# Performance work log

Hardware: AMD Instinct MI355X
Metric: run time of the kernel (lower is better)

Reference implementation:

```python
import jax, jax.numpy as jnp
import numpy as np

N_NODES = 50000
N_EDGES = 800000
D_FEAT = 64


def setup_inputs() -> dict:
    key = jax.random.key(0)
    k_x, k_e, k_w = jax.random.split(key, 3)
    x = jax.random.normal(k_x, (N_NODES, D_FEAT), dtype=jnp.float32)
    edge_index = jax.random.randint(k_e, (2, N_EDGES), 0, N_NODES, dtype=jnp.int64)
    # message MLP params (phi_Theta): single linear + ReLU
    W = jax.random.normal(k_w, (D_FEAT, D_FEAT), dtype=jnp.float32) / np.sqrt(D_FEAT)
    b = jnp.zeros((D_FEAT,), dtype=jnp.float32)
    return {"x": x, "edge_index": edge_index, "W": W, "b": b}


def reference(x, edge_index, W, b):
    # flow = source_to_target: messages flow from edge_index[0] (j) to edge_index[1] (i)
    src = edge_index[0]  # j: source nodes (gather)
    dst = edge_index[1]  # i: target nodes (scatter index)
    n_nodes = x.shape[0]
    # __collect__: index_select gather of source node features -> x_j [E, D]
    x_j = x[src]
    # message: per-edge MLP  phi(x_j) = relu(x_j W + b)
    msg = jax.nn.relu(jnp.einsum('ed,df->ef', x_j, W) + b)
    # aggregate: scatter-add into target nodes (aggr='add', dim_size = size_i)
    out = jax.ops.segment_sum(msg, dst, num_segments=n_nodes)
    # update: identity
    return out
```

## Files before the change

### kernel.cpp

```cpp
#include <hip/hip_runtime.h>
#include <hip/hip_bf16.h>

#define D 64
#define CAP 32
#define OVF_CAP 16384
#define TROWS 64


__device__ __forceinline__ float bf2f(unsigned short u) {
    return __uint_as_float((unsigned int)u << 16);
}
__device__ __forceinline__ unsigned short f2bf(float f) {
    unsigned int u = __float_as_uint(f);
    unsigned int r = (u + 0x7fffu + ((u >> 16) & 1u)) >> 16;
    return (unsigned short)r;
}

__global__ __launch_bounds__(256) void node_mlp_lds_kernel(
    const float* __restrict__ x, const float* __restrict__ W,
    const float* __restrict__ b, unsigned short* __restrict__ m,
    int* __restrict__ cnt, int* __restrict__ ovf_cnt, int n_nodes) {
    __shared__ float tile[TROWS][68];
    for (int i = blockIdx.x * blockDim.x + threadIdx.x; i < n_nodes;
         i += gridDim.x * blockDim.x) cnt[i] = 0;
    if (blockIdx.x == 0 && threadIdx.x == 0) *ovf_cnt = 0;

    const int lane = threadIdx.x & 63;
    const int wv = threadIdx.x >> 6;
    float w[D];
    #pragma unroll
    for (int k = 0; k < D; ++k) w[k] = W[k * D + lane];
    const float bias = b[lane];

    for (int t0 = blockIdx.x * TROWS; t0 < n_nodes; t0 += gridDim.x * TROWS) {
        const int nr = min(TROWS, n_nodes - t0);
        {
            const int r = threadIdx.x >> 2, sg = threadIdx.x & 3;
            if (r < nr) {
                const float4* s4 = (const float4*)(x + (size_t)(t0 + r) * D + sg * 16);
                float4 a0 = s4[0], a1 = s4[1], a2 = s4[2], a3 = s4[3];
                float* dl = &tile[r][sg * 16];
                *(float4*)(dl + 0)  = a0;
                *(float4*)(dl + 4)  = a1;
                *(float4*)(dl + 8)  = a2;
                *(float4*)(dl + 12) = a3;
            }
        }
        __syncthreads();
        const int rend = min(wv * 16 + 16, nr);
        for (int rr = wv * 16; rr < rend; rr += 2) {
            const int r0 = rr;
            const int r1 = (rr + 1 < rend) ? rr + 1 : rr;
            float acc0 = bias, acc1 = bias;
            #pragma unroll
            for (int kk = 0; kk < D / 4; ++kk) {
                float4 a = *(const float4*)&tile[r0][4 * kk];
                float4 c = *(const float4*)&tile[r1][4 * kk];
                acc0 = fmaf(a.x, w[4 * kk + 0], acc0);
                acc1 = fmaf(c.x, w[4 * kk + 0], acc1);
                acc0 = fmaf(a.y, w[4 * kk + 1], acc0);
                acc1 = fmaf(c.y, w[4 * kk + 1], acc1);
                acc0 = fmaf(a.z, w[4 * kk + 2], acc0);
                acc1 = fmaf(c.z, w[4 * kk + 2], acc1);
                acc0 = fmaf(a.w, w[4 * kk + 3], acc0);
                acc1 = fmaf(c.w, w[4 * kk + 3], acc1);
            }
            m[(size_t)(t0 + r0) * D + lane] = f2bf(fmaxf(acc0, 0.0f));
            if (r1 > r0)
                m[(size_t)(t0 + r1) * D + lane] = f2bf(fmaxf(acc1, 0.0f));
        }
        __syncthreads();
    }
}

__global__ __launch_bounds__(256) void append_kernel(
    const int* __restrict__ src, const int* __restrict__ dst,
    int* __restrict__ cnt, unsigned short* __restrict__ slots,
    int* __restrict__ ovf_cnt, unsigned int* __restrict__ ovf,
    int n_edges) {
    const int stride = gridDim.x * 256;
    for (int e = blockIdx.x * 256 + (int)threadIdx.x; e < n_edges; e += stride) {
        int d = dst[e];
        int s = src[e];
        int pos = atomicAdd(&cnt[d], 1);
        if (pos < CAP) {
            slots[(size_t)d * CAP + pos] = (unsigned short)s;
        } else {
            int op = atomicAdd(ovf_cnt, 1);
            if (op < OVF_CAP)
                ovf[op] = ((unsigned int)d << 16) | (unsigned int)s;
        }
    }
}

__global__ __launch_bounds__(256) void gather_kernel(
    const unsigned short* __restrict__ slots, const int* __restrict__ cnt,
    const unsigned short* __restrict__ m,
    const int* __restrict__ ovf_cnt, const unsigned int* __restrict__ ovf,
    float* __restrict__ out, int n_nodes) {
    const int grp = blockIdx.x >> 3;
    const int xcd = blockIdx.x & 7;
    int node = grp * 32 + ((threadIdx.x >> 6) << 3) + xcd;
    if (node >= n_nodes) return;
    node = __builtin_amdgcn_readfirstlane(node);

    const int lane = threadIdx.x & 63;

    const int c = cnt[node];
    const int cc = min(c, CAP);
    const unsigned int* __restrict__ row =
        (const unsigned int*)(slots + (size_t)node * CAP);

    float acc = 0.0f;
    int k = 0;
    for (; k + 16 <= cc; k += 16) {
        unsigned int p[8];
        #pragma unroll
        for (int i = 0; i < 8; ++i) p[i] = row[(k >> 1) + i];
        float v[16];
        #pragma unroll
        for (int i = 0; i < 8; ++i) {
            const unsigned short* ba = m + (size_t)(p[i] & 0xFFFFu) * D;
            const unsigned short* bb = m + (size_t)(p[i] >> 16) * D;
            v[2 * i + 0] = bf2f(ba[lane]);
            v[2 * i + 1] = bf2f(bb[lane]);
        }
        float t0 = ((v[0] + v[1]) + (v[2] + v[3])) + ((v[4] + v[5]) + (v[6] + v[7]));
        float t1 = ((v[8] + v[9]) + (v[10] + v[11])) + ((v[12] + v[13]) + (v[14] + v[15]));
        acc += t0 + t1;
    }
    for (; k + 4 <= cc; k += 4) {
        unsigned int p0 = row[(k >> 1) + 0];
        unsigned int p1 = row[(k >> 1) + 1];
        const unsigned short* b0 = m + (size_t)(p0 & 0xFFFFu) * D;
        const unsigned short* b1 = m + (size_t)(p0 >> 16) * D;
        const unsigned short* b2 = m + (size_t)(p1 & 0xFFFFu) * D;
        const unsigned short* b3 = m + (size_t)(p1 >> 16) * D;
        float v0 = bf2f(b0[lane]);
        float v1 = bf2f(b1[lane]);
        float v2 = bf2f(b2[lane]);
        float v3 = bf2f(b3[lane]);
        acc += (v0 + v1) + (v2 + v3);
    }
    for (; k < cc; ++k) {
        unsigned int p = row[k >> 1];
        unsigned int s = (k & 1) ? (p >> 16) : (p & 0xFFFFu);
        acc += bf2f(m[(size_t)s * D + lane]);
    }
    if (c > CAP) {
        int oc = min(*ovf_cnt, OVF_CAP);
        for (int i = 0; i < oc; ++i) {
            unsigned int e = ovf[i];
            if ((int)(e >> 16) == node)
                acc += bf2f(m[(size_t)(e & 0xFFFFu) * D + lane]);
        }
    }
    out[(size_t)node * D + lane] = acc;
}

__global__ __launch_bounds__(256) void edge_scatter_kernel(
    const int* __restrict__ src, const int* __restrict__ dst,
    const unsigned short* __restrict__ m, float* __restrict__ out, int n_edges) {
    long long t = (long long)blockIdx.x * blockDim.x + threadIdx.x;
    int e = (int)(t >> 4);
    if (e >= n_edges) return;
    int c = (int)(t & 15) << 2;
    int s = src[e];
    int d = dst[e];
    const ushort4 v = *(const ushort4*)(m + (size_t)s * D + c);
    float* o = out + (size_t)d * D + c;
    atomicAdd(o + 0, bf2f(v.x));
    atomicAdd(o + 1, bf2f(v.y));
    atomicAdd(o + 2, bf2f(v.z));
    atomicAdd(o + 3, bf2f(v.w));
}

static inline size_t align_up(size_t v, size_t a) { return (v + a - 1) & ~(a - 1); }

extern "C" void kernel_launch(void* const* d_in, const int* in_sizes, int n_in,
                              void* d_out, int out_size, void* d_ws, size_t ws_size,
                              hipStream_t stream) {
    const float* x = (const float*)d_in[0];
    const int* edge_index = (const int*)d_in[1];
    const float* W = (const float*)d_in[2];
    const float* b = (const float*)d_in[3];
    float* out = (float*)d_out;

    const int n_nodes = in_sizes[0] / D;
    const int n_edges = in_sizes[1] / 2;
    const int* src = edge_index;
    const int* dst = edge_index + n_edges;

    size_t off = 0;
    unsigned short* m = (unsigned short*)((char*)d_ws + off);
    off = align_up(off + (size_t)n_nodes * D * sizeof(unsigned short), 256);
    int* cnt = (int*)((char*)d_ws + off);
    off = align_up(off + (size_t)n_nodes * sizeof(int), 256);
    unsigned short* slots = (unsigned short*)((char*)d_ws + off);
    off = align_up(off + (size_t)n_nodes * CAP * sizeof(unsigned short), 256);
    int* ovf_cnt = (int*)((char*)d_ws + off);
    off = align_up(off + sizeof(int), 256);
    unsigned int* ovf = (unsigned int*)((char*)d_ws + off);
    off = align_up(off + (size_t)OVF_CAP * sizeof(unsigned int), 256);
    const size_t needed = off;

    const int mlp_blocks = (n_nodes + TROWS - 1) / TROWS;
    node_mlp_lds_kernel<<<mlp_blocks, 256, 0, stream>>>(x, W, b, m, cnt, ovf_cnt, n_nodes);

    if (ws_size >= needed && n_nodes <= 65536) {
        const int app_blocks = (n_edges + 255) / 256;
        append_kernel<<<app_blocks, 256, 0, stream>>>(
            src, dst, cnt, slots, ovf_cnt, ovf, n_edges);
        const int ngroups = (n_nodes + 31) / 32;
        gather_kernel<<<ngroups * 8, 256, 0, stream>>>(
            slots, cnt, m, ovf_cnt, ovf, out, n_nodes);
    } else {
        hipMemsetAsync(d_out, 0, (size_t)out_size * sizeof(float), stream);
        long long total_threads = (long long)n_edges * 16;
        int scat_blocks = (int)((total_threads + 255) / 256);
        edge_scatter_kernel<<<scat_blocks, 256, 0, stream>>>(src, dst, m, out, n_edges);
    }
}
```

Baseline: 150.5 us.

## Shard append kernel by destination node modulo XCD count

The append kernel is restructured so each block handles one of eight destination shards (dst mod 8), matching the blockIdx-to-XCD mapping. The goal is to keep the atomics on cnt and the slot writes for a node inside one XCD's L2, avoiding cross-die coherence traffic. It also unrolls four edges per thread so more atomics are in flight at once. The cost is that every shard reads the whole dst array, which multiplies index reads by eight, and each thread gets fewer useful edges.

```diff
diff --git a/kernel.cpp b/kernel.cpp
--- a/kernel.cpp
+++ b/kernel.cpp
@@ -4,6 +4,7 @@
 #define D 64
 #define CAP 32
 #define OVF_CAP 16384
+#define NSHARD 8
 #define TROWS 64
 
 
@@ -77,18 +78,39 @@
     const int* __restrict__ src, const int* __restrict__ dst,
     int* __restrict__ cnt, unsigned short* __restrict__ slots,
     int* __restrict__ ovf_cnt, unsigned int* __restrict__ ovf,
-    int n_edges) {
-    const int stride = gridDim.x * 256;
-    for (int e = blockIdx.x * 256 + (int)threadIdx.x; e < n_edges; e += stride) {
-        int d = dst[e];
-        int s = src[e];
-        int pos = atomicAdd(&cnt[d], 1);
-        if (pos < CAP) {
-            slots[(size_t)d * CAP + pos] = (unsigned short)s;
-        } else {
-            int op = atomicAdd(ovf_cnt, 1);
-            if (op < OVF_CAP)
-                ovf[op] = ((unsigned int)d << 16) | (unsigned int)s;
+    int n_edges, int blocks_per_shard) {
+    const int shard = blockIdx.x & (NSHARD - 1);
+    const int p = blockIdx.x >> 3;
+    const int chunk = (n_edges + blocks_per_shard - 1) / blocks_per_shard;
+    const int beg = p * chunk;
+    const int end = min(beg + chunk, n_edges);
+
+    for (int e0 = beg + (int)threadIdx.x; e0 < end; e0 += 256 * 4) {
+        int  dd[4], ss[4];
+        bool mm[4];
+        #pragma unroll
+        for (int u = 0; u < 4; ++u) {
+            const int e = e0 + u * 256;
+            const bool valid = (e < end);
+            const int d = valid ? dst[e] : 0;
+            mm[u] = valid && ((d & (NSHARD - 1)) == shard);
+            dd[u] = d;
+            ss[u] = mm[u] ? src[e] : 0;
+        }
+        int pos[4];
+        #pragma unroll
+        for (int u = 0; u < 4; ++u)
+            if (mm[u]) pos[u] = atomicAdd(&cnt[dd[u]], 1);
+        #pragma unroll
+        for (int u = 0; u < 4; ++u) {
+            if (!mm[u]) continue;
+            if (pos[u] < CAP) {
+                slots[(size_t)dd[u] * CAP + pos[u]] = (unsigned short)ss[u];
+            } else {
+                int op = atomicAdd(ovf_cnt, 1);
+                if (op < OVF_CAP)
+                    ovf[op] = ((unsigned int)dd[u] << 16) | (unsigned int)ss[u];
+            }
         }
     }
 }
@@ -208,9 +230,9 @@
     node_mlp_lds_kernel<<<mlp_blocks, 256, 0, stream>>>(x, W, b, m, cnt, ovf_cnt, n_nodes);
 
     if (ws_size >= needed && n_nodes <= 65536) {
-        const int app_blocks = (n_edges + 255) / 256;
-        append_kernel<<<app_blocks, 256, 0, stream>>>(
-            src, dst, cnt, slots, ovf_cnt, ovf, n_edges);
+        const int blocks_per_shard = 320;
+        append_kernel<<<blocks_per_shard * NSHARD, 256, 0, stream>>>(
+            src, dst, cnt, slots, ovf_cnt, ovf, n_edges, blocks_per_shard);
         const int ngroups = (n_nodes + 31) / 32;
         gather_kernel<<<ngroups * 8, 256, 0, stream>>>(
             slots, cnt, m, ovf_cnt, ovf, out, n_nodes);
```

Measured after the change: 144.2 us. 1.04x faster.

## Shard edge append by destination XCD and retile node MLP to 32 rows

Applied to the files above, without the earlier changes.

The append kernel now assigns each block to a shard (blockIdx & 7), matching the round-robin block-to-XCD dispatch. Each block scans a chunk of edges and keeps only those whose destination node falls in its shard, so the atomics and slot writes for a node stay within one XCD's L2. The price is that every edge's dst is read 8 times across shards. The node MLP separately switches to 32-row tiles with 4 rows per wave iteration, giving more blocks and more ILP per wave.

```diff
diff --git a/kernel.cpp b/kernel.cpp
--- a/kernel.cpp
+++ b/kernel.cpp
@@ -4,7 +4,8 @@
 #define D 64
 #define CAP 32
 #define OVF_CAP 16384
-#define TROWS 64
+#define NSHARD 8
+#define TROWS 32
 
 
 __device__ __forceinline__ float bf2f(unsigned short u) {
@@ -35,39 +36,50 @@
     for (int t0 = blockIdx.x * TROWS; t0 < n_nodes; t0 += gridDim.x * TROWS) {
         const int nr = min(TROWS, n_nodes - t0);
         {
-            const int r = threadIdx.x >> 2, sg = threadIdx.x & 3;
+            const int r = threadIdx.x >> 3, sg = threadIdx.x & 7;
             if (r < nr) {
-                const float4* s4 = (const float4*)(x + (size_t)(t0 + r) * D + sg * 16);
-                float4 a0 = s4[0], a1 = s4[1], a2 = s4[2], a3 = s4[3];
-                float* dl = &tile[r][sg * 16];
-                *(float4*)(dl + 0)  = a0;
-                *(float4*)(dl + 4)  = a1;
-                *(float4*)(dl + 8)  = a2;
-                *(float4*)(dl + 12) = a3;
+                const float4* s4 = (const float4*)(x + (size_t)(t0 + r) * D + sg * 8);
+                float4 a0 = s4[0], a1 = s4[1];
+                float* dl = &tile[r][sg * 8];
+                *(float4*)(dl + 0) = a0;
+                *(float4*)(dl + 4) = a1;
             }
         }
         __syncthreads();
-        const int rend = min(wv * 16 + 16, nr);
-        for (int rr = wv * 16; rr < rend; rr += 2) {
+        const int rend = min(wv * 8 + 8, nr);
+        for (int rr = wv * 8; rr < rend; rr += 4) {
             const int r0 = rr;
-            const int r1 = (rr + 1 < rend) ? rr + 1 : rr;
-            float acc0 = bias, acc1 = bias;
+            const int r1 = min(rr + 1, rend - 1);
+            const int r2 = min(rr + 2, rend - 1);
+            const int r3 = min(rr + 3, rend - 1);
+            float acc0 = bias, acc1 = bias, acc2 = bias, acc3 = bias;
             #pragma unroll
             for (int kk = 0; kk < D / 4; ++kk) {
                 float4 a = *(const float4*)&tile[r0][4 * kk];
                 float4 c = *(const float4*)&tile[r1][4 * kk];
+                float4 e = *(const float4*)&tile[r2][4 * kk];
+                float4 g = *(const float4*)&tile[r3][4 * kk];
                 acc0 = fmaf(a.x, w[4 * kk + 0], acc0);
                 acc1 = fmaf(c.x, w[4 * kk + 0], acc1);
+                acc2 = fmaf(e.x, w[4 * kk + 0], acc2);
+                acc3 = fmaf(g.x, w[4 * kk + 0], acc3);
                 acc0 = fmaf(a.y, w[4 * kk + 1], acc0);
                 acc1 = fmaf(c.y, w[4 * kk + 1], acc1);
+                acc2 = fmaf(e.y, w[4 * kk + 1], acc2);
+                acc3 = fmaf(g.y, w[4 * kk + 1], acc3);
                 acc0 = fmaf(a.z, w[4 * kk + 2], acc0);
                 acc1 = fmaf(c.z, w[4 * kk + 2], acc1);
+                acc2 = fmaf(e.z, w[4 * kk + 2], acc2);
+                acc3 = fmaf(g.z, w[4 * kk + 2], acc3);
                 acc0 = fmaf(a.w, w[4 * kk + 3], acc0);
                 acc1 = fmaf(c.w, w[4 * kk + 3], acc1);
+                acc2 = fmaf(e.w, w[4 * kk + 3], acc2);
+                acc3 = fmaf(g.w, w[4 * kk + 3], acc3);
             }
             m[(size_t)(t0 + r0) * D + lane] = f2bf(fmaxf(acc0, 0.0f));
-            if (r1 > r0)
-                m[(size_t)(t0 + r1) * D + lane] = f2bf(fmaxf(acc1, 0.0f));
+            if (rr + 1 < rend) m[(size_t)(t0 + r1) * D + lane] = f2bf(fmaxf(acc1, 0.0f));
+            if (rr + 2 < rend) m[(size_t)(t0 + r2) * D + lane] = f2bf(fmaxf(acc2, 0.0f));
+            if (rr + 3 < rend) m[(size_t)(t0 + r3) * D + lane] = f2bf(fmaxf(acc3, 0.0f));
         }
         __syncthreads();
     }
@@ -77,10 +89,16 @@
     const int* __restrict__ src, const int* __restrict__ dst,
     int* __restrict__ cnt, unsigned short* __restrict__ slots,
     int* __restrict__ ovf_cnt, unsigned int* __restrict__ ovf,
-    int n_edges) {
-    const int stride = gridDim.x * 256;
-    for (int e = blockIdx.x * 256 + (int)threadIdx.x; e < n_edges; e += stride) {
+    int n_edges, int blocks_per_shard) {
+    const int shard = blockIdx.x & (NSHARD - 1);
+    const int p = blockIdx.x >> 3;
+    const int chunk = (n_edges + blocks_per_shard - 1) / blocks_per_shard;
+    const int beg = p * chunk;
+    const int end = min(beg + chunk, n_edges);
+
+    for (int e = beg + (int)threadIdx.x; e < end; e += 256) {
         int d = dst[e];
+        if ((d & (NSHARD - 1)) != shard) continue;
         int s = src[e];
         int pos = atomicAdd(&cnt[d], 1);
         if (pos < CAP) {
@@ -208,9 +226,9 @@
     node_mlp_lds_kernel<<<mlp_blocks, 256, 0, stream>>>(x, W, b, m, cnt, ovf_cnt, n_nodes);
 
     if (ws_size >= needed && n_nodes <= 65536) {
-        const int app_blocks = (n_edges + 255) / 256;
-        append_kernel<<<app_blocks, 256, 0, stream>>>(
-            src, dst, cnt, slots, ovf_cnt, ovf, n_edges);
+        const int blocks_per_shard = 320;
+        append_kernel<<<blocks_per_shard * NSHARD, 256, 0, stream>>>(
+            src, dst, cnt, slots, ovf_cnt, ovf, n_edges, blocks_per_shard);
         const int ngroups = (n_nodes + 31) / 32;
         gather_kernel<<<ngroups * 8, 256, 0, stream>>>(
             slots, cnt, m, ovf_cnt, ovf, out, n_nodes);
```

Result: slower. 154.0 us (+2.3%).
